# Kernel tuning notes

Measured on AMD Instinct MI355X. Metric: run time of the kernel, lower is better.

Reference implementation:

```python
import jax, jax.numpy as jnp
import numpy as np

N, E = 50000, 800000
H_IN, H, L = 256, 128, 3
EPS = 1e-5  # BatchNorm1d default eps


def setup_inputs() -> dict:
    key = jax.random.key(0)
    ks = jax.random.split(key, 8)
    x = jax.random.normal(ks[0], (N, H_IN), jnp.float32)
    edge_index = jax.random.randint(ks[1], (2, E), 0, N, dtype=jnp.int32)

    def glorot(k, fi, fo):
        lim = np.sqrt(6.0 / (fi + fo)).astype(np.float32)
        return jax.random.uniform(k, (fi, fo), jnp.float32, -lim, lim)

    W_feat = glorot(ks[2], H_IN, H)
    b_feat = jnp.zeros((H,), jnp.float32)
    wkeys = jax.random.split(ks[3], L)
    Ws = jnp.stack([glorot(wkeys[i], H, H) for i in range(L)])
    bs = jnp.zeros((L, H), jnp.float32)
    # BN init per reset_parameters: weight=1, bias=1e-4
    bn_feat_g = jnp.ones((H_IN,), jnp.float32)
    bn_feat_b = jnp.full((H_IN,), 1e-4, jnp.float32)
    bn_g = jnp.ones((L, H), jnp.float32)
    bn_b = jnp.full((L, H), 1e-4, jnp.float32)
    return dict(x=x, edge_index=edge_index, bn_feat_g=bn_feat_g, bn_feat_b=bn_feat_b,
                W_feat=W_feat, b_feat=b_feat, bn_g=bn_g, bn_b=bn_b, Ws=Ws, bs=bs)


def _bn(x, gamma, beta):
    # training-mode BatchNorm1d: batch statistics over nodes, biased variance
    mu = x.mean(0)
    var = x.var(0)
    return (x - mu) * jax.lax.rsqrt(var + EPS) * gamma + beta


def _gcn_norm(edge_index, n):
    # add self-loops (fill value 1) + symmetric deg^-1/2 normalization
    row, col = edge_index[0], edge_index[1]
    loop = jnp.arange(n, dtype=row.dtype)
    row = jnp.concatenate([row, loop])
    col = jnp.concatenate([col, loop])
    deg = jax.ops.segment_sum(jnp.ones_like(row, jnp.float32), row, num_segments=n)
    dinv = jnp.where(deg > 0, jax.lax.rsqrt(deg), 0.0)
    return row, col, dinv[row] * dinv[col]


def _gcn(x, W, b, row, col, norm, n):
    x = x @ W                                   # [n, out]
    msg = x[row] * norm[:, None]                # gather + scale, [E+n, out]
    out = jax.ops.segment_sum(msg, col, num_segments=n)  # scatter-add
    return out + b


def reference(x, edge_index, bn_feat_g, bn_feat_b, W_feat, b_feat, bn_g, bn_b, Ws, bs):
    n = x.shape[0]
    row, col, norm = _gcn_norm(edge_index, n)   # same for every layer
    x = _bn(x, bn_feat_g, bn_feat_b)
    x = _gcn(x, W_feat, b_feat, row, col, norm, n)
    for i in range(L):
        x = _bn(x, bn_g[i], bn_b[i])
        x = _gcn(x, Ws[i], bs[i], row, col, norm, n)
    return x
```

## Files before the change

kernel.cpp:

```cpp
#include <hip/hip_runtime.h>
#include <hip/hip_bf16.h>

#define H_IN 256
#define H    128
#define BN_EPS 1e-5f
#define NCOPY 32
#define NSLICE 256
#define SMAX 5120
#define STATS_FLOATS (NCOPY * 2 * H_IN)

using u16 = unsigned short;
using u32 = unsigned int;
typedef __attribute__((ext_vector_type(8))) unsigned short us8;
typedef __attribute__((ext_vector_type(8))) short bf16x8;
typedef __attribute__((ext_vector_type(4))) float f32x4;

__device__ __forceinline__ float b2f(u16 u) {
    return __uint_as_float(((u32)u) << 16);
}
__device__ __forceinline__ u16 f2b(float f) {
    u32 u = __float_as_uint(f);
    u += 0x7FFF + ((u >> 16) & 1);
    return (u16)(u >> 16);
}

__global__ __launch_bounds__(256) void radix1_k(const int* __restrict__ row,
                                                const int* __restrict__ col,
                                                u32* __restrict__ hist_part,
                                                u32* __restrict__ bcnt_part,
                                                int E, int halfN, int hwords) {
    extern __shared__ u32 lds[];
    u32* hist = lds;
    u32* bcnt = lds + hwords;
    int tid = threadIdx.x;
    int slice = blockIdx.x >> 1;
    int half = blockIdx.x & 1;
    for (int i = tid; i < hwords; i += 256) hist[i] = 0;
    bcnt[tid] = 0;
    __syncthreads();

    int len = (E + NSLICE - 1) / NSLICE;
    int e0 = slice * len;
    int e1 = min(e0 + len, E);
    int lo = half * halfN;
    for (int e = e0 + tid; e < e1; e += 256) {
        int r = row[e] - lo;
        if ((u32)r < (u32)halfN)
            atomicAdd(&hist[r >> 1], 1u << ((r & 1) << 4));
        if (half == 0) atomicAdd(&bcnt[((u32)col[e]) >> 8], 1u);
    }
    __syncthreads();
    u32* hdst = hist_part + (size_t)blockIdx.x * hwords;
    for (int i = tid; i < hwords; i += 256) hdst[i] = hist[i];
    if (half == 0) bcnt_part[slice * 256 + tid] = bcnt[tid];
}

#define ZB 64
__global__ __launch_bounds__(256) void mid_k(const u32* __restrict__ bcnt_part,
                                             u32* __restrict__ boff,
                                             u32* __restrict__ btot,
                                             const u32* __restrict__ hist_part,
                                             float* __restrict__ dinv,
                                             float* __restrict__ stats_mc,
                                             int N, int halfN, int hwords) {
    int b = blockIdx.x;
    int tid = threadIdx.x;
    if (b < 256) {
        __shared__ u32 sh[256];
        u32 v = bcnt_part[tid * 256 + b];
        sh[tid] = v;
        __syncthreads();
        for (int o = 1; o < 256; o <<= 1) {
            u32 x = (tid >= o) ? sh[tid - o] : 0;
            __syncthreads();
            sh[tid] += x;
            __syncthreads();
        }
        boff[tid * 256 + b] = sh[tid] - v;
        if (tid == 255) btot[b] = sh[255];
    } else if (b < 256 + ZB) {
        int i = (b - 256) * 256 + tid;
        if (i < STATS_FLOATS) stats_mc[i] = 0.f;
    } else {
        int w = (b - 256 - ZB) * 256 + tid;
        if (w >= 2 * hwords) return;
        int h = (w >= hwords) ? 1 : 0;
        int lw = w - h * hwords;
        u32 v = 0;
        for (int s = 0; s < NSLICE; ++s) v += hist_part[(size_t)(s * 2 + h) * hwords + lw];
        int n = h * halfN + 2 * lw;
        if (n < N)     dinv[n]     = rsqrtf((float)(v & 0xFFFF) + 1.0f);
        if (n + 1 < N) dinv[n + 1] = rsqrtf((float)(v >> 16) + 1.0f);
    }
}

__global__ void scanb_b_k(const u32* __restrict__ btot, u32* __restrict__ bbase) {
    __shared__ u32 sh[256];
    int k = threadIdx.x;
    u32 v = btot[k];
    sh[k] = v;
    __syncthreads();
    for (int o = 1; o < 256; o <<= 1) {
        u32 x = (k >= o) ? sh[k - o] : 0;
        __syncthreads();
        sh[k] += x;
        __syncthreads();
    }
    bbase[k] = sh[k] - v;
    if (k == 255) bbase[256] = sh[255];
}

__global__ __launch_bounds__(256) void scat2_k(const int* __restrict__ row,
                                               const int* __restrict__ col,
                                               const u32* __restrict__ boff,
                                               const u32* __restrict__ bbase,
                                               u32* __restrict__ ebuf, int E) {
    __shared__ u32 cur[256];
    int tid = threadIdx.x;
    int slice = blockIdx.x;
    cur[tid] = boff[slice * 256 + tid] + bbase[tid];
    __syncthreads();
    int len = (E + NSLICE - 1) / NSLICE;
    int e0 = slice * len;
    int e1 = min(e0 + len, E);
    for (int e = e0 + tid; e < e1; e += 256) {
        u32 r = (u32)row[e];
        u32 c = (u32)col[e];
        u32 pos = atomicAdd(&cur[c >> 8], 1u);
        ebuf[pos] = r | ((c & 255u) << 16);
    }
}

__global__ __launch_bounds__(256) void sortb_k(const u32* __restrict__ ebuf,
                                               const u32* __restrict__ bbase,
                                               int* __restrict__ rowptr,
                                               u16* __restrict__ esrc, int N) {
    __shared__ u32 est[SMAX];
    __shared__ u32 hist[256], scanv[256], cur[256];
    int b = blockIdx.x, tid = threadIdx.x;
    u32 base = bbase[b];
    int size = (int)(bbase[b + 1] - base);
    int st = min(size, SMAX);
    hist[tid] = 0;
    __syncthreads();
    for (int i = tid; i < st; i += 256) {
        u32 e = ebuf[base + i];
        est[i] = e;
        atomicAdd(&hist[(e >> 16) & 255u], 1u);
    }
    for (int i = SMAX + tid; i < size; i += 256) {
        u32 e = ebuf[base + i];
        atomicAdd(&hist[(e >> 16) & 255u], 1u);
    }
    __syncthreads();
    u32 own = hist[tid];
    scanv[tid] = own;
    __syncthreads();
    for (int o = 1; o < 256; o <<= 1) {
        u32 t = (tid >= o) ? scanv[tid - o] : 0;
        __syncthreads();
        scanv[tid] += t;
        __syncthreads();
    }
    u32 excl = scanv[tid] - own;
    int idx = (b << 8) + tid;
    if (idx <= N) rowptr[idx] = (int)(base + excl);
    cur[tid] = excl;
    __syncthreads();
    for (int i = tid; i < st; i += 256) {
        u32 e = est[i];
        u32 pos = atomicAdd(&cur[(e >> 16) & 255u], 1u);
        esrc[base + pos] = (u16)(e & 0xFFFFu);
    }
    for (int i = SMAX + tid; i < size; i += 256) {
        u32 e = ebuf[base + i];
        u32 pos = atomicAdd(&cur[(e >> 16) & 255u], 1u);
        esrc[base + pos] = (u16)(e & 0xFFFFu);
    }
}

__global__ __launch_bounds__(256) void stats0_k(const float* __restrict__ A,
                                                u16* __restrict__ xb,
                                                float* __restrict__ stats_mc,
                                                int total4, int K) {
    __shared__ float sh[2 * H_IN];
    int tid = threadIdx.x;
    int csz = 2 * K;
    sh[tid] = 0.f;
    sh[tid + 256] = 0.f;
    __syncthreads();
    int gid = blockIdx.x * 256 + tid;
    int stride = gridDim.x * 256;
    int c0 = (gid * 4) % K;
    float s0=0.f,s1=0.f,s2=0.f,s3=0.f, q0=0.f,q1=0.f,q2=0.f,q3=0.f;
    const float4* A4 = (const float4*)A;
    ushort4* X4 = (ushort4*)xb;
    for (int i = gid; i < total4; i += stride) {
        float4 v = A4[i];
        ushort4 xv;
        xv.x = f2b(v.x); xv.y = f2b(v.y); xv.z = f2b(v.z); xv.w = f2b(v.w);
        X4[i] = xv;
        s0 += v.x; q0 += v.x * v.x;
        s1 += v.y; q1 += v.y * v.y;
        s2 += v.z; q2 += v.z * v.z;
        s3 += v.w; q3 += v.w * v.w;
    }
    atomicAdd(&sh[c0],     s0); atomicAdd(&sh[K + c0],     q0);
    atomicAdd(&sh[c0 + 1], s1); atomicAdd(&sh[K + c0 + 1], q1);
    atomicAdd(&sh[c0 + 2], s2); atomicAdd(&sh[K + c0 + 2], q2);
    atomicAdd(&sh[c0 + 3], s3); atomicAdd(&sh[K + c0 + 3], q3);
    __syncthreads();
    float* dst = stats_mc + (size_t)(blockIdx.x & (NCOPY - 1)) * csz;
    for (int i = tid; i < csz; i += 256) atomicAdd(&dst[i], sh[i]);
}

__global__ void fold_k(const float* __restrict__ W, const float* __restrict__ stats_mc,
                       const float* __restrict__ g, const float* __restrict__ b,
                       const float* __restrict__ bias, u16* __restrict__ Wt,
                       float* __restrict__ bp, int N, int K) {
    int j = blockIdx.x;
    int k = threadIdx.x;
    int csz = 2 * K;
    float sum = 0.f, sumsq = 0.f;
#pragma unroll
    for (int c = 0; c < NCOPY; ++c) {
        sum   += stats_mc[(size_t)c * csz + k];
        sumsq += stats_mc[(size_t)c * csz + K + k];
    }
    float mu = sum / (float)N;
    float var = sumsq / (float)N - mu * mu;
    float s = g[k] * rsqrtf(var + BN_EPS);
    float t = b[k] - mu * s;
    float w = W[(size_t)k * H + j];
    Wt[(size_t)j * K + k] = f2b(s * w);
    __shared__ float red[256];
    red[k] = t * w;
    __syncthreads();
    for (int o = blockDim.x >> 1; o > 0; o >>= 1) {
        if (k < o) red[k] += red[k + o];
        __syncthreads();
    }
    if (k == 0) bp[j] = bias[j] + red[0];
}

template<int KT>
__global__ __launch_bounds__(256) void gemm_mfma_k(const u16* __restrict__ Ab,
                                                   const u16* __restrict__ Wt,
                                                   u16* __restrict__ Yb, int M,
                                                   float* __restrict__ stats_z) {
    const int K = KT * 32;
    int tid = threadIdx.x;
    if (stats_z && blockIdx.x == 0) {
        for (int i = tid; i < STATS_FLOATS; i += 256) stats_z[i] = 0.f;
    }
    int w = tid >> 6;
    int lane = tid & 63;
    int m16 = lane & 15;
    int q = lane >> 4;

    bf16x8 bfrag[KT][2];
#pragma unroll
    for (int t = 0; t < KT; ++t)
#pragma unroll
        for (int p = 0; p < 2; ++p) {
            int ncol = 32 * w + 16 * p + m16;
            bfrag[t][p] = *(const bf16x8*)(Wt + (size_t)ncol * K + 32 * t + 8 * q);
        }

    int nchunk = M >> 4;
    for (int c = blockIdx.x; c < nchunk; c += gridDim.x) {
        int m0 = c << 4;
        const u16* Arow = Ab + (size_t)(m0 + m16) * K + 8 * q;
        bf16x8 afrag[KT];
#pragma unroll
        for (int t = 0; t < KT; ++t)
            afrag[t] = *(const bf16x8*)(Arow + 32 * t);
        f32x4 acc0 = {0.f, 0.f, 0.f, 0.f}, acc1 = {0.f, 0.f, 0.f, 0.f};
#pragma unroll
        for (int t = 0; t < KT; ++t) {
            acc0 = __builtin_amdgcn_mfma_f32_16x16x32_bf16(afrag[t], bfrag[t][0], acc0, 0, 0, 0);
            acc1 = __builtin_amdgcn_mfma_f32_16x16x32_bf16(afrag[t], bfrag[t][1], acc1, 0, 0, 0);
        }
        u16* Crow = Yb + (size_t)(m0 + q * 4) * H + 32 * w + m16;
#pragma unroll
        for (int i = 0; i < 4; ++i) {
            Crow[(size_t)i * H]      = f2b(acc0[i]);
            Crow[(size_t)i * H + 16] = f2b(acc1[i]);
        }
    }
}

__global__ __launch_bounds__(256) void csragg_k(const int* __restrict__ rowptr,
                                                const u16* __restrict__ esrc,
                                                const u16* __restrict__ Yb,
                                                const float* __restrict__ dinv,
                                                const float* __restrict__ bp,
                                                u16* __restrict__ Ob,
                                                float* __restrict__ Of,
                                                float* __restrict__ stats_mc,
                                                int do_stats, int N) {
    __shared__ float sh[1024];
    int tid = threadIdx.x;
    int node = blockIdx.x * 16 + (tid >> 4);
    int fl = tid & 15;
    float o[8] = {0.f,0.f,0.f,0.f,0.f,0.f,0.f,0.f};
    if (node < N) {
        const us8* Y8 = (const us8*)Yb;
        float dn = dinv[node];
        float acc[8];
        {
            us8 ys = Y8[(size_t)node * 16 + fl];
#pragma unroll
            for (int j = 0; j < 8; ++j) acc[j] = dn * b2f(ys[j]);
        }
        int s = rowptr[node], e = rowptr[node + 1];
        int p = s;
        for (; p + 3 < e; p += 4) {
            int s0 = esrc[p], s1 = esrc[p + 1], s2 = esrc[p + 2], s3 = esrc[p + 3];
            float n0 = dinv[s0], n1 = dinv[s1], n2 = dinv[s2], n3 = dinv[s3];
            us8 v0 = Y8[(size_t)s0 * 16 + fl];
            us8 v1 = Y8[(size_t)s1 * 16 + fl];
            us8 v2 = Y8[(size_t)s2 * 16 + fl];
            us8 v3 = Y8[(size_t)s3 * 16 + fl];
#pragma unroll
            for (int j = 0; j < 8; ++j) acc[j] += n0 * b2f(v0[j]);
#pragma unroll
            for (int j = 0; j < 8; ++j) acc[j] += n1 * b2f(v1[j]);
#pragma unroll
            for (int j = 0; j < 8; ++j) acc[j] += n2 * b2f(v2[j]);
#pragma unroll
            for (int j = 0; j < 8; ++j) acc[j] += n3 * b2f(v3[j]);
        }
        for (; p < e; ++p) {
            int s0 = esrc[p];
            float n0 = dinv[s0];
            us8 v0 = Y8[(size_t)s0 * 16 + fl];
#pragma unroll
            for (int j = 0; j < 8; ++j) acc[j] += n0 * b2f(v0[j]);
        }
        float4 b0 = ((const float4*)bp)[fl * 2];
        float4 b1 = ((const float4*)bp)[fl * 2 + 1];
        o[0] = b0.x + dn * acc[0]; o[1] = b0.y + dn * acc[1];
        o[2] = b0.z + dn * acc[2]; o[3] = b0.w + dn * acc[3];
        o[4] = b1.x + dn * acc[4]; o[5] = b1.y + dn * acc[5];
        o[6] = b1.z + dn * acc[6]; o[7] = b1.w + dn * acc[7];
        if (Of) {
            float4* O4 = (float4*)Of;
            O4[(size_t)node * 32 + fl * 2]     = make_float4(o[0], o[1], o[2], o[3]);
            O4[(size_t)node * 32 + fl * 2 + 1] = make_float4(o[4], o[5], o[6], o[7]);
        } else {
            us8 ov;
#pragma unroll
            for (int j = 0; j < 8; ++j) ov[j] = f2b(o[j]);
            *(us8*)(Ob + (size_t)node * H + fl * 8) = ov;
        }
    }
    if (do_stats) {
        float sv[16];
#pragma unroll
        for (int j = 0; j < 8; ++j) { sv[j] = o[j]; sv[8 + j] = o[j] * o[j]; }
#pragma unroll
        for (int j = 0; j < 16; ++j) {
            sv[j] += __shfl_xor(sv[j], 16, 64);
            sv[j] += __shfl_xor(sv[j], 32, 64);
        }
        int lane = tid & 63, wv = tid >> 6;
        if (lane < 16) {
            float* base = sh + wv * 256;
#pragma unroll
            for (int j = 0; j < 8; ++j) {
                base[fl * 8 + j]       = sv[j];
                base[128 + fl * 8 + j] = sv[8 + j];
            }
        }
        __syncthreads();
        float v = sh[tid] + sh[256 + tid] + sh[512 + tid] + sh[768 + tid];
        atomicAdd(&stats_mc[(size_t)(blockIdx.x & (NCOPY - 1)) * (2 * H) + tid], v);
    }
}

extern "C" void kernel_launch(void* const* d_in, const int* in_sizes, int n_in,
                              void* d_out, int out_size, void* d_ws, size_t ws_size,
                              hipStream_t stream) {
    const float* x     = (const float*)d_in[0];
    const int*   ei    = (const int*)d_in[1];
    const float* bnfg  = (const float*)d_in[2];
    const float* bnfb  = (const float*)d_in[3];
    const float* Wfeat = (const float*)d_in[4];
    const float* bfeat = (const float*)d_in[5];
    const float* bng   = (const float*)d_in[6];
    const float* bnb   = (const float*)d_in[7];
    const float* Ws    = (const float*)d_in[8];
    const float* bs    = (const float*)d_in[9];

    int N = in_sizes[0] / H_IN;
    int E = in_sizes[1] / 2;
    const int* row = ei;
    const int* col = ei + E;

    int halfN  = (N + 1) / 2;
    int hwords = (halfN + 1) / 2;
    int NB     = (N + 255) >> 8;

    char* p = (char*)d_ws;
    auto alloc = [&](size_t bytes) { char* r = p; p += (bytes + 63) & ~size_t(63); return r; };
    float* dinv      = (float*)alloc(N * 4);
    float* stats_mc  = (float*)alloc(STATS_FLOATS * 4);
    u16*   Wt        = (u16*)alloc(H_IN * H * 2);
    float* bp        = (float*)alloc(H * 4);
    u32*   hist_part = (u32*)alloc((size_t)NSLICE * 2 * hwords * 4);
    u32*   bcnt_part = (u32*)alloc(NSLICE * 256 * 4);
    u32*   boff      = (u32*)alloc(NSLICE * 256 * 4);
    u32*   btot      = (u32*)alloc(256 * 4);
    u32*   bbase     = (u32*)alloc(260 * 4);
    int*   rowptr    = (int*)alloc((N + 1) * 4);
    u32*   ebuf      = (u32*)alloc((size_t)E * 4);
    u16*   esrc      = (u16*)alloc((size_t)E * 2);
    u16*   xb        = (u16*)alloc((size_t)N * H_IN * 2);
    u16*   Yb        = (u16*)alloc((size_t)N * H * 2);
    u16*   ACTb      = (u16*)alloc((size_t)N * H * 2);

    float* out = (float*)d_out;

    size_t r1_lds = (size_t)(hwords + 256) * 4;
    radix1_k<<<2 * NSLICE, 256, r1_lds, stream>>>(row, col, hist_part, bcnt_part, E, halfN, hwords);
    int dblocks = (2 * hwords + 255) / 256;
    mid_k<<<256 + ZB + dblocks, 256, 0, stream>>>(bcnt_part, boff, btot, hist_part,
                                                  dinv, stats_mc, N, halfN, hwords);
    scanb_b_k<<<1, 256, 0, stream>>>(btot, bbase);
    scat2_k<<<NSLICE, 256, 0, stream>>>(row, col, boff, bbase, ebuf, E);
    sortb_k<<<NB, 256, 0, stream>>>(ebuf, bbase, rowptr, esrc, N);

    stats0_k<<<512, 256, 0, stream>>>(x, xb, stats_mc, N * H_IN / 4, H_IN);

    for (int l = 0; l < 4; ++l) {
        const u16* Ab     = (l == 0) ? xb : ACTb;
        int K             = (l == 0) ? H_IN : H;
        const float* W    = (l == 0) ? Wfeat : Ws + (size_t)(l - 1) * H * H;
        const float* bias = (l == 0) ? bfeat : bs + (size_t)(l - 1) * H;
        const float* g    = (l == 0) ? bnfg : bng + (size_t)(l - 1) * H;
        const float* bb   = (l == 0) ? bnfb : bnb + (size_t)(l - 1) * H;
        int do_stats      = (l < 3);

        fold_k<<<H, K, 0, stream>>>(W, stats_mc, g, bb, bias, Wt, bp, N, K);
        float* sz = do_stats ? stats_mc : nullptr;
        if (l == 0) gemm_mfma_k<8><<<512, 256, 0, stream>>>(Ab, Wt, Yb, N, sz);
        else        gemm_mfma_k<4><<<512, 256, 0, stream>>>(Ab, Wt, Yb, N, sz);
        csragg_k<<<(N + 15) / 16, 256, 0, stream>>>(rowptr, esrc, Yb, dinv, bp,
                                                    ACTb, (l == 3) ? out : nullptr,
                                                    stats_mc, do_stats, N);
    }
}
```

Before: 380.6 us.

## Fuse graph preprocessing kernels and overlap sort with first GEMM

Collapses the radix-histogram, scan, scatter and stats kernels into two multi-role launches. Degrees now come from direct global atomics instead of per-slice packed histograms. The bucket sort runs as extra blocks inside the first GEMM launch, and BN stats use ping-pong buffers zeroed by a memset. The aim is fewer launches and less idle time between dependent small kernels, at the cost of global atomic contention on deg and redundant per-block prefix reads of bcnt_part.

```diff
diff --git a/kernel.cpp b/kernel.cpp
--- a/kernel.cpp
+++ b/kernel.cpp
@@ -8,6 +8,8 @@
 #define NSLICE 256
 #define SMAX 5120
 #define STATS_FLOATS (NCOPY * 2 * H_IN)
+#define SBLK 512
+#define GEMMB 512
 
 using u16 = unsigned short;
 using u32 = unsigned int;
@@ -24,194 +26,141 @@
     return (u16)(u >> 16);
 }
 
-__global__ __launch_bounds__(256) void radix1_k(const int* __restrict__ row,
-                                                const int* __restrict__ col,
-                                                u32* __restrict__ hist_part,
-                                                u32* __restrict__ bcnt_part,
-                                                int E, int halfN, int hwords) {
-    extern __shared__ u32 lds[];
-    u32* hist = lds;
-    u32* bcnt = lds + hwords;
+__global__ __launch_bounds__(256) void build_k(const int* __restrict__ row,
+                                               const int* __restrict__ col,
+                                               u32* __restrict__ deg,
+                                               u32* __restrict__ bcnt_part,
+                                               const float* __restrict__ x,
+                                               u16* __restrict__ xb,
+                                               float* __restrict__ statsA,
+                                               int E, int total4) {
     int tid = threadIdx.x;
-    int slice = blockIdx.x >> 1;
-    int half = blockIdx.x & 1;
-    for (int i = tid; i < hwords; i += 256) hist[i] = 0;
-    bcnt[tid] = 0;
-    __syncthreads();
-
-    int len = (E + NSLICE - 1) / NSLICE;
-    int e0 = slice * len;
-    int e1 = min(e0 + len, E);
-    int lo = half * halfN;
-    for (int e = e0 + tid; e < e1; e += 256) {
-        int r = row[e] - lo;
-        if ((u32)r < (u32)halfN)
-            atomicAdd(&hist[r >> 1], 1u << ((r & 1) << 4));
-        if (half == 0) atomicAdd(&bcnt[((u32)col[e]) >> 8], 1u);
-    }
-    __syncthreads();
-    u32* hdst = hist_part + (size_t)blockIdx.x * hwords;
-    for (int i = tid; i < hwords; i += 256) hdst[i] = hist[i];
-    if (half == 0) bcnt_part[slice * 256 + tid] = bcnt[tid];
-}
-
-#define ZB 64
-__global__ __launch_bounds__(256) void mid_k(const u32* __restrict__ bcnt_part,
-                                             u32* __restrict__ boff,
-                                             u32* __restrict__ btot,
-                                             const u32* __restrict__ hist_part,
-                                             float* __restrict__ dinv,
-                                             float* __restrict__ stats_mc,
-                                             int N, int halfN, int hwords) {
-    int b = blockIdx.x;
+    if (blockIdx.x < NSLICE) {
+        __shared__ u32 bcnt[256];
+        bcnt[tid] = 0;
+        __syncthreads();
+        int len = (E + NSLICE - 1) / NSLICE;
+        int e0 = blockIdx.x * len;
+        int e1 = min(e0 + len, E);
+        for (int e = e0 + tid; e < e1; e += 256) {
+            atomicAdd(&deg[(u32)row[e]], 1u);
+            atomicAdd(&bcnt[((u32)col[e]) >> 8], 1u);
+        }
+        __syncthreads();
+        bcnt_part[blockIdx.x * 256 + tid] = bcnt[tid];
+    } else {
+        __shared__ float sh[2 * H_IN];
+        const int K = H_IN;
+        const int csz = 2 * H_IN;
+        sh[tid] = 0.f;
+        sh[tid + 256] = 0.f;
+        __syncthreads();
+        int gid = (blockIdx.x - NSLICE) * 256 + tid;
+        int stride = SBLK * 256;
+        int c0 = (gid * 4) % K;
+        float s0=0.f,s1=0.f,s2=0.f,s3=0.f, q0=0.f,q1=0.f,q2=0.f,q3=0.f;
+        const float4* A4 = (const float4*)x;
+        ushort4* X4 = (ushort4*)xb;
+        for (int i = gid; i < total4; i += stride) {
+            float4 v = A4[i];
+            ushort4 xv;
+            xv.x = f2b(v.x); xv.y = f2b(v.y); xv.z = f2b(v.z); xv.w = f2b(v.w);
+            X4[i] = xv;
+            s0 += v.x; q0 += v.x * v.x;
+            s1 += v.y; q1 += v.y * v.y;
+            s2 += v.z; q2 += v.z * v.z;
+            s3 += v.w; q3 += v.w * v.w;
+        }
+        atomicAdd(&sh[c0],     s0); atomicAdd(&sh[K + c0],     q0);
+        atomicAdd(&sh[c0 + 1], s1); atomicAdd(&sh[K + c0 + 1], q1);
+        atomicAdd(&sh[c0 + 2], s2); atomicAdd(&sh[K + c0 + 2], q2);
+        atomicAdd(&sh[c0 + 3], s3); atomicAdd(&sh[K + c0 + 3], q3);
+        __syncthreads();
+        float* dst = statsA + (size_t)((blockIdx.x - NSLICE) & (NCOPY - 1)) * csz;
+        for (int i = tid; i < csz; i += 256) atomicAdd(&dst[i], sh[i]);
+    }
+}
+
+__global__ __launch_bounds__(256) void prep_k(const int* __restrict__ row,
+                                              const int* __restrict__ col,
+                                              const u32* __restrict__ bcnt_part,
+                                              u32* __restrict__ bbase,
+                                              u32* __restrict__ ebuf,
+                                              const u32* __restrict__ deg,
+                                              float* __restrict__ dinv,
+                                              const float* __restrict__ W,
+                                              const float* __restrict__ stats_mc,
+                                              const float* __restrict__ g,
+                                              const float* __restrict__ bcoef,
+                                              const float* __restrict__ bias,
+                                              u16* __restrict__ Wt,
+                                              float* __restrict__ bp,
+                                              int E, int N, int DB) {
     int tid = threadIdx.x;
-    if (b < 256) {
-        __shared__ u32 sh[256];
-        u32 v = bcnt_part[tid * 256 + b];
-        sh[tid] = v;
+    int bx = blockIdx.x;
+    if (bx < NSLICE) {
+        __shared__ u32 sc[256];
+        __shared__ u32 cur[256];
+        int s = bx;
+        u32 tot = 0, pre = 0;
+        for (int t = 0; t < NSLICE; ++t) {
+            u32 v = bcnt_part[t * 256 + tid];
+            tot += v;
+            if (t < s) pre += v;
+        }
+        sc[tid] = tot;
         __syncthreads();
         for (int o = 1; o < 256; o <<= 1) {
-            u32 x = (tid >= o) ? sh[tid - o] : 0;
-            __syncthreads();
-            sh[tid] += x;
-            __syncthreads();
-        }
-        boff[tid * 256 + b] = sh[tid] - v;
-        if (tid == 255) btot[b] = sh[255];
-    } else if (b < 256 + ZB) {
-        int i = (b - 256) * 256 + tid;
-        if (i < STATS_FLOATS) stats_mc[i] = 0.f;
+            u32 xv = (tid >= o) ? sc[tid - o] : 0;
+            __syncthreads();
+            sc[tid] += xv;
+            __syncthreads();
+        }
+        u32 base = sc[tid] - tot;
+        if (s == 0) {
+            bbase[tid] = base;
+            if (tid == 255) bbase[256] = sc[255];
+        }
+        cur[tid] = base + pre;
+        __syncthreads();
+        int len = (E + NSLICE - 1) / NSLICE;
+        int e0 = s * len;
+        int e1 = min(e0 + len, E);
+        for (int e = e0 + tid; e < e1; e += 256) {
+            u32 r = (u32)row[e];
+            u32 c = (u32)col[e];
+            u32 pos = atomicAdd(&cur[c >> 8], 1u);
+            ebuf[pos] = r | ((c & 255u) << 16);
+        }
+    } else if (bx < NSLICE + DB) {
+        int n = (bx - NSLICE) * 256 + tid;
+        if (n < N) dinv[n] = rsqrtf((float)deg[n] + 1.0f);
     } else {
-        int w = (b - 256 - ZB) * 256 + tid;
-        if (w >= 2 * hwords) return;
-        int h = (w >= hwords) ? 1 : 0;
-        int lw = w - h * hwords;
-        u32 v = 0;
-        for (int s = 0; s < NSLICE; ++s) v += hist_part[(size_t)(s * 2 + h) * hwords + lw];
-        int n = h * halfN + 2 * lw;
-        if (n < N)     dinv[n]     = rsqrtf((float)(v & 0xFFFF) + 1.0f);
-        if (n + 1 < N) dinv[n + 1] = rsqrtf((float)(v >> 16) + 1.0f);
-    }
-}
-
-__global__ void scanb_b_k(const u32* __restrict__ btot, u32* __restrict__ bbase) {
-    __shared__ u32 sh[256];
-    int k = threadIdx.x;
-    u32 v = btot[k];
-    sh[k] = v;
-    __syncthreads();
-    for (int o = 1; o < 256; o <<= 1) {
-        u32 x = (k >= o) ? sh[k - o] : 0;
-        __syncthreads();
-        sh[k] += x;
-        __syncthreads();
-    }
-    bbase[k] = sh[k] - v;
-    if (k == 255) bbase[256] = sh[255];
-}
-
-__global__ __launch_bounds__(256) void scat2_k(const int* __restrict__ row,
-                                               const int* __restrict__ col,
-                                               const u32* __restrict__ boff,
-                                               const u32* __restrict__ bbase,
-                                               u32* __restrict__ ebuf, int E) {
-    __shared__ u32 cur[256];
-    int tid = threadIdx.x;
-    int slice = blockIdx.x;
-    cur[tid] = boff[slice * 256 + tid] + bbase[tid];
-    __syncthreads();
-    int len = (E + NSLICE - 1) / NSLICE;
-    int e0 = slice * len;
-    int e1 = min(e0 + len, E);
-    for (int e = e0 + tid; e < e1; e += 256) {
-        u32 r = (u32)row[e];
-        u32 c = (u32)col[e];
-        u32 pos = atomicAdd(&cur[c >> 8], 1u);
-        ebuf[pos] = r | ((c & 255u) << 16);
-    }
-}
-
-__global__ __launch_bounds__(256) void sortb_k(const u32* __restrict__ ebuf,
-                                               const u32* __restrict__ bbase,
-                                               int* __restrict__ rowptr,
-                                               u16* __restrict__ esrc, int N) {
-    __shared__ u32 est[SMAX];
-    __shared__ u32 hist[256], scanv[256], cur[256];
-    int b = blockIdx.x, tid = threadIdx.x;
-    u32 base = bbase[b];
-    int size = (int)(bbase[b + 1] - base);
-    int st = min(size, SMAX);
-    hist[tid] = 0;
-    __syncthreads();
-    for (int i = tid; i < st; i += 256) {
-        u32 e = ebuf[base + i];
-        est[i] = e;
-        atomicAdd(&hist[(e >> 16) & 255u], 1u);
-    }
-    for (int i = SMAX + tid; i < size; i += 256) {
-        u32 e = ebuf[base + i];
-        atomicAdd(&hist[(e >> 16) & 255u], 1u);
-    }
-    __syncthreads();
-    u32 own = hist[tid];
-    scanv[tid] = own;
-    __syncthreads();
-    for (int o = 1; o < 256; o <<= 1) {
-        u32 t = (tid >= o) ? scanv[tid - o] : 0;
-        __syncthreads();
-        scanv[tid] += t;
-        __syncthreads();
-    }
-    u32 excl = scanv[tid] - own;
-    int idx = (b << 8) + tid;
-    if (idx <= N) rowptr[idx] = (int)(base + excl);
-    cur[tid] = excl;
-    __syncthreads();
-    for (int i = tid; i < st; i += 256) {
-        u32 e = est[i];
-        u32 pos = atomicAdd(&cur[(e >> 16) & 255u], 1u);
-        esrc[base + pos] = (u16)(e & 0xFFFFu);
-    }
-    for (int i = SMAX + tid; i < size; i += 256) {
-        u32 e = ebuf[base + i];
-        u32 pos = atomicAdd(&cur[(e >> 16) & 255u], 1u);
-        esrc[base + pos] = (u16)(e & 0xFFFFu);
-    }
-}
-
-__global__ __launch_bounds__(256) void stats0_k(const float* __restrict__ A,
-                                                u16* __restrict__ xb,
-                                                float* __restrict__ stats_mc,
-                                                int total4, int K) {
-    __shared__ float sh[2 * H_IN];
-    int tid = threadIdx.x;
-    int csz = 2 * K;
-    sh[tid] = 0.f;
-    sh[tid + 256] = 0.f;
-    __syncthreads();
-    int gid = blockIdx.x * 256 + tid;
-    int stride = gridDim.x * 256;
-    int c0 = (gid * 4) % K;
-    float s0=0.f,s1=0.f,s2=0.f,s3=0.f, q0=0.f,q1=0.f,q2=0.f,q3=0.f;
-    const float4* A4 = (const float4*)A;
-    ushort4* X4 = (ushort4*)xb;
-    for (int i = gid; i < total4; i += stride) {
-        float4 v = A4[i];
-        ushort4 xv;
-        xv.x = f2b(v.x); xv.y = f2b(v.y); xv.z = f2b(v.z); xv.w = f2b(v.w);
-        X4[i] = xv;
-        s0 += v.x; q0 += v.x * v.x;
-        s1 += v.y; q1 += v.y * v.y;
-        s2 += v.z; q2 += v.z * v.z;
-        s3 += v.w; q3 += v.w * v.w;
-    }
-    atomicAdd(&sh[c0],     s0); atomicAdd(&sh[K + c0],     q0);
-    atomicAdd(&sh[c0 + 1], s1); atomicAdd(&sh[K + c0 + 1], q1);
-    atomicAdd(&sh[c0 + 2], s2); atomicAdd(&sh[K + c0 + 2], q2);
-    atomicAdd(&sh[c0 + 3], s3); atomicAdd(&sh[K + c0 + 3], q3);
-    __syncthreads();
-    float* dst = stats_mc + (size_t)(blockIdx.x & (NCOPY - 1)) * csz;
-    for (int i = tid; i < csz; i += 256) atomicAdd(&dst[i], sh[i]);
+        int j = bx - NSLICE - DB;
+        int k = tid;
+        const int K = H_IN;
+        const int csz = 2 * H_IN;
+        float sum = 0.f, sumsq = 0.f;
+#pragma unroll
+        for (int c = 0; c < NCOPY; ++c) {
+            sum   += stats_mc[(size_t)c * csz + k];
+            sumsq += stats_mc[(size_t)c * csz + K + k];
+        }
+        float mu = sum / (float)N;
+        float var = sumsq / (float)N - mu * mu;
+        float sK = g[k] * rsqrtf(var + BN_EPS);
+        float tK = bcoef[k] - mu * sK;
+        float w = W[(size_t)k * H + j];
+        Wt[(size_t)j * K + k] = f2b(sK * w);
+        __shared__ float red[256];
+        red[k] = tK * w;
+        __syncthreads();
+        for (int o = 128; o > 0; o >>= 1) {
+            if (k < o) red[k] += red[k + o];
+            __syncthreads();
+        }
+        if (k == 0) bp[j] = bias[j] + red[0];
+    }
 }
 
 __global__ void fold_k(const float* __restrict__ W, const float* __restrict__ stats_mc,
@@ -243,13 +192,64 @@
     if (k == 0) bp[j] = bias[j] + red[0];
 }
 
-template<int KT>
+template<int KT, int WITH_SORT>
 __global__ __launch_bounds__(256) void gemm_mfma_k(const u16* __restrict__ Ab,
                                                    const u16* __restrict__ Wt,
                                                    u16* __restrict__ Yb, int M,
-                                                   float* __restrict__ stats_z) {
+                                                   float* __restrict__ stats_z,
+                                                   const u32* __restrict__ ebuf,
+                                                   const u32* __restrict__ bbase,
+                                                   int* __restrict__ rowptr,
+                                                   u16* __restrict__ esrc, int N) {
+    int tid = threadIdx.x;
+    if constexpr (WITH_SORT != 0) {
+        if (blockIdx.x >= GEMMB) {
+            __shared__ u32 est[SMAX];
+            __shared__ u32 hist[256], scanv[256], cur[256];
+            int b = blockIdx.x - GEMMB;
+            u32 base = bbase[b];
+            int size = (int)(bbase[b + 1] - base);
+            int st = min(size, SMAX);
+            hist[tid] = 0;
+            __syncthreads();
+            for (int i = tid; i < st; i += 256) {
+                u32 e = ebuf[base + i];
+                est[i] = e;
+                atomicAdd(&hist[(e >> 16) & 255u], 1u);
+            }
+            for (int i = SMAX + tid; i < size; i += 256) {
+                u32 e = ebuf[base + i];
+                atomicAdd(&hist[(e >> 16) & 255u], 1u);
+            }
+            __syncthreads();
+            u32 own = hist[tid];
+            scanv[tid] = own;
+            __syncthreads();
+            for (int o = 1; o < 256; o <<= 1) {
+                u32 t = (tid >= o) ? scanv[tid - o] : 0;
+                __syncthreads();
+                scanv[tid] += t;
+                __syncthreads();
+            }
+            u32 excl = scanv[tid] - own;
+            int idx = (b << 8) + tid;
+            if (idx <= N) rowptr[idx] = (int)(base + excl);
+            cur[tid] = excl;
+            __syncthreads();
+            for (int i = tid; i < st; i += 256) {
+                u32 e = est[i];
+                u32 pos = atomicAdd(&cur[(e >> 16) & 255u], 1u);
+                esrc[base + pos] = (u16)(e & 0xFFFFu);
+            }
+            for (int i = SMAX + tid; i < size; i += 256) {
+                u32 e = ebuf[base + i];
+                u32 pos = atomicAdd(&cur[(e >> 16) & 255u], 1u);
+                esrc[base + pos] = (u16)(e & 0xFFFFu);
+            }
+            return;
+        }
+    }
     const int K = KT * 32;
-    int tid = threadIdx.x;
     if (stats_z && blockIdx.x == 0) {
         for (int i = tid; i < STATS_FLOATS; i += 256) stats_z[i] = 0.f;
     }
@@ -268,7 +268,7 @@
         }
 
     int nchunk = M >> 4;
-    for (int c = blockIdx.x; c < nchunk; c += gridDim.x) {
+    for (int c = blockIdx.x; c < nchunk; c += GEMMB) {
         int m0 = c << 4;
         const u16* Arow = Ab + (size_t)(m0 + m16) * K + 8 * q;
         bf16x8 afrag[KT];
@@ -398,22 +398,19 @@
     const int* row = ei;
     const int* col = ei + E;
 
-    int halfN  = (N + 1) / 2;
-    int hwords = (halfN + 1) / 2;
-    int NB     = (N + 255) >> 8;
+    int NB = (N + 255) >> 8;
 
     char* p = (char*)d_ws;
     auto alloc = [&](size_t bytes) { char* r = p; p += (bytes + 63) & ~size_t(63); return r; };
-    float* dinv      = (float*)alloc(N * 4);
-    float* stats_mc  = (float*)alloc(STATS_FLOATS * 4);
+    float* statsA    = (float*)alloc(STATS_FLOATS * 4);
+    float* statsB    = (float*)alloc(STATS_FLOATS * 4);
+    u32*   deg       = (u32*)alloc((size_t)N * 4);
+    float* dinv      = (float*)alloc((size_t)N * 4);
     u16*   Wt        = (u16*)alloc(H_IN * H * 2);
     float* bp        = (float*)alloc(H * 4);
-    u32*   hist_part = (u32*)alloc((size_t)NSLICE * 2 * hwords * 4);
     u32*   bcnt_part = (u32*)alloc(NSLICE * 256 * 4);
-    u32*   boff      = (u32*)alloc(NSLICE * 256 * 4);
-    u32*   btot      = (u32*)alloc(256 * 4);
-    u32*   bbase     = (u32*)alloc(260 * 4);
-    int*   rowptr    = (int*)alloc((N + 1) * 4);
+    u32*   bbase     = (u32*)alloc(257 * 4);
+    int*   rowptr    = (int*)alloc((size_t)(N + 1) * 4);
     u32*   ebuf      = (u32*)alloc((size_t)E * 4);
     u16*   esrc      = (u16*)alloc((size_t)E * 2);
     u16*   xb        = (u16*)alloc((size_t)N * H_IN * 2);
@@ -422,32 +419,32 @@
 
     float* out = (float*)d_out;
 
-    size_t r1_lds = (size_t)(hwords + 256) * 4;
-    radix1_k<<<2 * NSLICE, 256, r1_lds, stream>>>(row, col, hist_part, bcnt_part, E, halfN, hwords);
-    int dblocks = (2 * hwords + 255) / 256;
-    mid_k<<<256 + ZB + dblocks, 256, 0, stream>>>(bcnt_part, boff, btot, hist_part,
-                                                  dinv, stats_mc, N, halfN, hwords);
-    scanb_b_k<<<1, 256, 0, stream>>>(btot, bbase);
-    scat2_k<<<NSLICE, 256, 0, stream>>>(row, col, boff, bbase, ebuf, E);
-    sortb_k<<<NB, 256, 0, stream>>>(ebuf, bbase, rowptr, esrc, N);
-
-    stats0_k<<<512, 256, 0, stream>>>(x, xb, stats_mc, N * H_IN / 4, H_IN);
-
-    for (int l = 0; l < 4; ++l) {
-        const u16* Ab     = (l == 0) ? xb : ACTb;
-        int K             = (l == 0) ? H_IN : H;
-        const float* W    = (l == 0) ? Wfeat : Ws + (size_t)(l - 1) * H * H;
-        const float* bias = (l == 0) ? bfeat : bs + (size_t)(l - 1) * H;
-        const float* g    = (l == 0) ? bnfg : bng + (size_t)(l - 1) * H;
-        const float* bb   = (l == 0) ? bnfb : bnb + (size_t)(l - 1) * H;
-        int do_stats      = (l < 3);
-
-        fold_k<<<H, K, 0, stream>>>(W, stats_mc, g, bb, bias, Wt, bp, N, K);
-        float* sz = do_stats ? stats_mc : nullptr;
-        if (l == 0) gemm_mfma_k<8><<<512, 256, 0, stream>>>(Ab, Wt, Yb, N, sz);
-        else        gemm_mfma_k<4><<<512, 256, 0, stream>>>(Ab, Wt, Yb, N, sz);
+    hipMemsetAsync(statsA, 0, (size_t)(2 * STATS_FLOATS) * 4 + (size_t)N * 4, stream);
+
+    build_k<<<NSLICE + SBLK, 256, 0, stream>>>(row, col, deg, bcnt_part, x, xb, statsA,
+                                               E, N * H_IN / 4);
+    prep_k<<<NSLICE + NB + H, 256, 0, stream>>>(row, col, bcnt_part, bbase, ebuf, deg, dinv,
+                                                Wfeat, statsA, bnfg, bnfb, bfeat, Wt, bp,
+                                                E, N, NB);
+    gemm_mfma_k<8, 1><<<GEMMB + NB, 256, 0, stream>>>(xb, Wt, Yb, N, nullptr,
+                                                      ebuf, bbase, rowptr, esrc, N);
+    csragg_k<<<(N + 15) / 16, 256, 0, stream>>>(rowptr, esrc, Yb, dinv, bp,
+                                                ACTb, nullptr, statsB, 1, N);
+
+    for (int l = 1; l < 4; ++l) {
+        const float* W    = Ws + (size_t)(l - 1) * H * H;
+        const float* bias = bs + (size_t)(l - 1) * H;
+        const float* g    = bng + (size_t)(l - 1) * H;
+        const float* bb   = bnb + (size_t)(l - 1) * H;
+        float* sfold   = (l & 1) ? statsB : statsA;
+        float* szero   = (l == 1) ? statsA : (l == 2) ? statsB : nullptr;
+        float* starget = ((l + 1) & 1) ? statsB : statsA;
+
+        fold_k<<<H, H, 0, stream>>>(W, sfold, g, bb, bias, Wt, bp, N, H);
+        gemm_mfma_k<4, 0><<<GEMMB, 256, 0, stream>>>(ACTb, Wt, Yb, N, szero,
+                                                     nullptr, nullptr, nullptr, nullptr, N);
         csragg_k<<<(N + 15) / 16, 256, 0, stream>>>(rowptr, esrc, Yb, dinv, bp,
                                                     ACTb, (l == 3) ? out : nullptr,
-                                                    stats_mc, do_stats, N);
-    }
-}
+                                                    starget, (l < 3) ? 1 : 0, N);
+    }
+}
```

Result: slower. 394.9 us (+3.7%).
